# Performance work log

Measured on AMD Instinct MI355X. Metric: run time of the kernel, lower is better.

Reference implementation:

```python
import jax, jax.numpy as jnp
import numpy as np

H_SIZE = 768
N_HEADS = 12
HEAD = H_SIZE // N_HEADS
INTER = 3072
N_LAYERS = 6
VOCAB = 65536
WIDTH = 512  # attention_width
EPS = 1e-6


def rmsnorm(x, w):
    return x * jax.lax.rsqrt(jnp.mean(x * x, axis=-1, keepdims=True) + EPS) * w


def rotate_every_two(x):
    # interleaved rotation: (x0,x1,x2,x3,...) -> (-x1,x0,-x3,x2,...)
    x1 = x[..., ::2]
    x2 = x[..., 1::2]
    return jnp.stack((-x2, x1), axis=-1).reshape(x.shape)


def fixed_pos_embedding(ages, dim):
    # ages: [B,S] float32 -> sin,cos: [B,S,1,dim]
    inv_freq = 1.0 / 10000 ** jnp.linspace(0.0, 2.0, dim // 2)
    t = ages[..., None] * inv_freq  # [B,S,dim//2]
    sin, cos = jnp.sin(t), jnp.cos(t)
    shp = ages.shape + (1, dim)
    sin = jnp.stack((sin, sin), axis=-1).reshape(shp)
    cos = jnp.stack((cos, cos), axis=-1).reshape(shp)
    return sin, cos


def local_attention(q, k, v, width):
    # causal local attention: query i attends to keys j with i-width < j <= i
    B, S, H, D = q.shape
    nb = S // width
    qb = q.reshape(B, nb, width, H, D)
    pad = ((0, 0), (width, 0), (0, 0), (0, 0))
    kp = jnp.pad(k, pad).reshape(B, nb + 1, width, H, D)
    vp = jnp.pad(v, pad).reshape(B, nb + 1, width, H, D)
    k2 = jnp.concatenate((kp[:, :-1], kp[:, 1:]), axis=2)  # [B,nb,2W,H,D]
    v2 = jnp.concatenate((vp[:, :-1], vp[:, 1:]), axis=2)
    scale = 1.0 / jnp.sqrt(jnp.asarray(D, q.dtype))
    scores = jnp.einsum('bnqhd,bnkhd->bnhqk', qb, k2) * scale
    qi = jnp.arange(width)[:, None]
    kj = jnp.arange(2 * width)[None, :]
    blk = jnp.arange(nb)[:, None, None]
    # global: i = b*W+qi, j = b*W - W + kj ; valid: j<=i, i-j<W, j>=0
    valid = (kj > qi) & (kj <= qi + width) & ((blk * width - width + kj) >= 0)
    scores = jnp.where(valid[None, :, None, :, :], scores, -jnp.inf)
    attn = jax.nn.softmax(scores, axis=-1)
    out = jnp.einsum('bnhqk,bnkhd->bnqhd', attn, v2)
    return out.reshape(B, S, H, D)


def encoder_layer(x, sin, cos, p):
    B, S, _ = x.shape
    xn = rmsnorm(x, p['norm_w'])
    qkv = (xn @ p['attn_W'] + p['attn_b']).reshape(B, S, 3, N_HEADS, HEAD)
    q = qkv[:, :, 0] * cos + rotate_every_two(qkv[:, :, 0]) * sin
    k = qkv[:, :, 1] * cos + rotate_every_two(qkv[:, :, 1]) * sin
    v = qkv[:, :, 2]
    attn = local_attention(q, k, v, WIDTH).reshape(B, S, H_SIZE)
    ff = jax.nn.gelu(xn @ p['in_W'] + p['in_b'], approximate=False)
    combined = jnp.concatenate((attn, ff), axis=-1)
    return combined @ p['out_W'] + p['out_b']


def setup_inputs() -> dict:
    key = jax.random.key(0)
    ks = jax.random.split(key, 10)
    B, S = 4, 2048
    std = 0.02
    tokens = jax.random.randint(ks[0], (B, S), 0, VOCAB, dtype=jnp.int64 if jax.config.jax_enable_x64 else jnp.int32)
    ages = jax.random.uniform(ks[1], (B, S), dtype=jnp.float32) * 1000.0
    embed = jax.random.normal(ks[2], (VOCAB, H_SIZE), jnp.float32) * std
    in_norm_w = jnp.ones((H_SIZE,), jnp.float32)
    out_norm_w = jnp.ones((H_SIZE,), jnp.float32)
    norm_w = jnp.ones((N_LAYERS, H_SIZE), jnp.float32)
    attn_W = jax.random.normal(ks[3], (N_LAYERS, H_SIZE, 3 * H_SIZE), jnp.float32) * std
    attn_b = jnp.zeros((N_LAYERS, 3 * H_SIZE), jnp.float32)
    in_W = jax.random.normal(ks[4], (N_LAYERS, H_SIZE, INTER), jnp.float32) * std
    in_b = jnp.zeros((N_LAYERS, INTER), jnp.float32)
    out_W = jax.random.normal(ks[5], (N_LAYERS, H_SIZE + INTER, H_SIZE), jnp.float32) * std
    out_b = jnp.zeros((N_LAYERS, H_SIZE), jnp.float32)
    return {'tokens': tokens, 'ages': ages, 'embed': embed,
            'in_norm_w': in_norm_w, 'out_norm_w': out_norm_w, 'norm_w': norm_w,
            'attn_W': attn_W, 'attn_b': attn_b, 'in_W': in_W, 'in_b': in_b,
            'out_W': out_W, 'out_b': out_b}


def reference(tokens, ages, embed, in_norm_w, out_norm_w, norm_w, attn_W, attn_b, in_W, in_b, out_W, out_b):
    x = embed[tokens]
    x = rmsnorm(x, in_norm_w)
    sin, cos = fixed_pos_embedding(ages, HEAD)
    params = {'norm_w': norm_w, 'attn_W': attn_W, 'attn_b': attn_b,
              'in_W': in_W, 'in_b': in_b, 'out_W': out_W, 'out_b': out_b}

    def step(h, p):
        return h + encoder_layer(h, sin, cos, p), None

    x, _ = jax.lax.scan(step, x, params)
    return rmsnorm(x, out_norm_w)
```

## Files before the change

### kernel.cpp

```cpp
#include <hip/hip_runtime.h>
#include <hip/hip_bf16.h>
#include <math.h>

#define H_SIZE 768
#define N_HEADS 12
#define HEAD 64
#define INTER 3072
#define N_LAYERS 6
#define BATCH 4
#define SEQ 2048
#define BS (BATCH*SEQ)
#define EPSV 1e-6f

typedef __attribute__((ext_vector_type(8))) short bf16x8;
typedef __attribute__((ext_vector_type(4))) float f32x4;
typedef unsigned short u16;

__device__ inline float bf2f(u16 v) {
    union { float f; unsigned u; } x; x.u = ((unsigned)v) << 16; return x.f;
}
__device__ inline u16 f2bf(float f) {
    union { float f; unsigned u; } x; x.f = f;
    unsigned u = x.u;
    return (u16)((u + 0x7FFFu + ((u >> 16) & 1u)) >> 16);
}

__device__ __forceinline__ void stage16(const u16* g, u16* ldsbase) {
    __builtin_amdgcn_global_load_lds((const __attribute__((address_space(1))) void*)g,
                                     (__attribute__((address_space(3))) void*)ldsbase,
                                     16, 0, 0);
}

__global__ void probe_kernel(const u16* __restrict__ embed, const int* __restrict__ tokens,
                             int* __restrict__ flags) {
    if (threadIdx.x == 0 && blockIdx.x == 0) {
        int good = 0, evenzero = 0;
        for (int i = 0; i < 128; i++) {
            u16 h = embed[i];
            int e = (h >> 7) & 0xFF;
            if (h == 0 || (e >= 87 && e <= 133)) good++;
            if ((i & 1) == 0 && h == 0) evenzero++;
        }
        flags[0] = (evenzero >= 48) ? 1 : ((good >= 110) ? 0 : 1);
        int z = 0;
        for (int i = 0; i < 64; i++) if (tokens[2 * i + 1] == 0) z++;
        flags[1] = (z >= 60) ? 1 : 0;
    }
}

__global__ __launch_bounds__(256) void sincos_kernel(const void* __restrict__ ages,
                                                     float* __restrict__ SIN,
                                                     float* __restrict__ COS,
                                                     const int* __restrict__ flags) {
    int idx = blockIdx.x * 256 + threadIdx.x;
    if (idx >= BS * 32) return;
    bool f32in = flags[0] != 0;
    int row = idx >> 5, f = idx & 31;
    float age = f32in ? ((const float*)ages)[row] : bf2f(((const u16*)ages)[row]);
    float inv = expf(-(2.0f * (float)f / 31.0f) * 9.210340371976184f);
    float t = age * inv;
    SIN[idx] = sinf(t);
    COS[idx] = cosf(t);
}

__global__ __launch_bounds__(256) void wtrans_kernel(const void* __restrict__ Wsrc,
                                                     u16* __restrict__ Wt,
                                                     int K, int N, size_t ltstride,
                                                     const int* __restrict__ flags) {
    __shared__ u16 tile[64][72];
    bool f32in = flags[0] != 0;
    int l = blockIdx.z;
    const float* W32 = (const float*)Wsrc + (size_t)l * K * N;
    const u16*   W16 = (const u16*)Wsrc + (size_t)l * K * N;
    u16* out = Wt + (size_t)l * ltstride;
    int k0 = blockIdx.y * 64, n0 = blockIdx.x * 64;
    int t = threadIdx.x;
    int kk = t >> 3, nn = (t & 7) * 8;
#pragma unroll
    for (int it = 0; it < 2; it++) {
        int kr = kk + it * 32;
        u16 tmp[8];
        if (f32in) {
            const float* src = W32 + (size_t)(k0 + kr) * N + n0 + nn;
            float4 f0 = *(const float4*)src, f1 = *(const float4*)(src + 4);
            tmp[0] = f2bf(f0.x); tmp[1] = f2bf(f0.y); tmp[2] = f2bf(f0.z); tmp[3] = f2bf(f0.w);
            tmp[4] = f2bf(f1.x); tmp[5] = f2bf(f1.y); tmp[6] = f2bf(f1.z); tmp[7] = f2bf(f1.w);
        } else {
            uint4 v = *(const uint4*)(W16 + (size_t)(k0 + kr) * N + n0 + nn);
            const u16* pv = (const u16*)&v;
#pragma unroll
            for (int i = 0; i < 8; i++) tmp[i] = pv[i];
        }
        *(uint4*)(&tile[kr][nn]) = *(const uint4*)tmp;
    }
    __syncthreads();
    int n = t >> 3, kq = (t & 7) * 8;
#pragma unroll
    for (int it = 0; it < 2; it++) {
        int nr = n + it * 32;
        u16 tmp[8];
#pragma unroll
        for (int i = 0; i < 8; i++) tmp[i] = tile[kq + i][nr];
        *(uint4*)(out + (size_t)(n0 + nr) * K + k0 + kq) = *(const uint4*)tmp;
    }
}

__global__ __launch_bounds__(256) void bias_conv_kernel(const void* __restrict__ ab,
                                                        const void* __restrict__ ib,
                                                        const void* __restrict__ ob,
                                                        u16* __restrict__ dst,
                                                        const int* __restrict__ flags) {
    int i = blockIdx.x * 256 + threadIdx.x;
    bool f32in = flags[0] != 0;
    const int A = 6 * 2304, B = 6 * 3072, C = 6 * 768;
    if (i < A) dst[i] = f32in ? f2bf(((const float*)ab)[i]) : ((const u16*)ab)[i];
    else if (i < A + B) { int j = i - A; dst[i] = f32in ? f2bf(((const float*)ib)[j]) : ((const u16*)ib)[j]; }
    else if (i < A + B + C) { int j = i - A - B; dst[i] = f32in ? f2bf(((const float*)ob)[j]) : ((const u16*)ob)[j]; }
}

__global__ __launch_bounds__(256) void embed_norm_kernel(const int* __restrict__ tokens,
                                                         const void* __restrict__ embed,
                                                         const void* __restrict__ wbase,
                                                         float* __restrict__ X,
                                                         const int* __restrict__ flags) {
    int row = blockIdx.x * 4 + (threadIdx.x >> 6);
    int lane = threadIdx.x & 63;
    bool f32in = flags[0] != 0;
    bool i64 = flags[1] != 0;
    int tok = i64 ? tokens[2 * row] : tokens[row];
    tok &= 65535;
    const u16* er16 = (const u16*)embed + (size_t)tok * H_SIZE;
    const float* er32 = (const float*)embed + (size_t)tok * H_SIZE;
    const u16* w16 = (const u16*)wbase;
    const float* w32 = (const float*)wbase;
    float v[12]; float ss = 0.f;
#pragma unroll
    for (int k = 0; k < 12; k++) {
        int i = lane + k * 64;
        float t = f32in ? er32[i] : bf2f(er16[i]);
        v[k] = t; ss += t * t;
    }
#pragma unroll
    for (int off = 1; off < 64; off <<= 1) ss += __shfl_xor(ss, off, 64);
    float scale = rsqrtf(ss * (1.0f / 768.0f) + EPSV);
#pragma unroll
    for (int k = 0; k < 12; k++) {
        int i = lane + k * 64;
        float wv = f32in ? w32[i] : bf2f(w16[i]);
        X[(size_t)row * H_SIZE + i] = v[k] * scale * wv;
    }
}

__global__ __launch_bounds__(256) void rmsnorm_kernel(const float* __restrict__ X,
                                                      const void* __restrict__ wbase, size_t woff,
                                                      void* __restrict__ Y, int outMode,
                                                      const int* __restrict__ flags) {
    int row = blockIdx.x * 4 + (threadIdx.x >> 6);
    int lane = threadIdx.x & 63;
    bool f32in = flags[0] != 0;
    const u16* w16 = (const u16*)wbase + woff;
    const float* w32 = (const float*)wbase + woff;
    const float* xr = X + (size_t)row * H_SIZE;
    float v[12]; float ss = 0.f;
#pragma unroll
    for (int k = 0; k < 12; k++) { v[k] = xr[lane + k * 64]; ss += v[k] * v[k]; }
#pragma unroll
    for (int off = 1; off < 64; off <<= 1) ss += __shfl_xor(ss, off, 64);
    float scale = rsqrtf(ss * (1.0f / 768.0f) + EPSV);
    bool of32 = outMode && f32in;
#pragma unroll
    for (int k = 0; k < 12; k++) {
        int i = lane + k * 64;
        float wv = f32in ? w32[i] : bf2f(w16[i]);
        float val = v[k] * scale * wv;
        if (of32) ((float*)Y)[(size_t)row * H_SIZE + i] = val;
        else      ((u16*)Y)[(size_t)row * H_SIZE + i] = f2bf(val);
    }
}

template <int EPI, int BN, int MGRP>
__global__ __launch_bounds__(256) void gemm_kernel(const u16* __restrict__ A,
                                                   const u16* __restrict__ Wt,
                                                   const u16* __restrict__ abias,
                                                   const u16* __restrict__ bbias,
                                                   float* __restrict__ Cf,
                                                   u16* __restrict__ qkvb,
                                                   u16* __restrict__ combb,
                                                   int K,
                                                   const float* __restrict__ SIN,
                                                   const float* __restrict__ COS) {
    constexpr int NF = BN / 32;
    constexpr int LPS = (BN == 128) ? 4 : 3;
    __shared__ u16 Al[3][128][32];
    __shared__ u16 Bl[3][BN][32];
    const int tid = threadIdx.x;
    const int lane = tid & 63, wave = tid >> 6;
    const int wm = wave >> 1, wn = wave & 1;
    const int lm = lane & 15, g = lane >> 4;

    const int nx = gridDim.x;
    const int mpx = gridDim.y >> 3;
    int linear = blockIdx.y * nx + blockIdx.x;
    const int xcd = linear & 7;
    int wch = linear >> 3;
    const int grpsz = MGRP * nx;
    int grp = wch / grpsz;
    int rem = wch - grp * grpsz;
    int n_idx = rem / MGRP;
    int m_loc = grp * MGRP + (rem - n_idx * MGRP);
    const int m0 = (xcd * mpx + m_loc) * 128;
    const int n0 = n_idx * BN;

    f32x4 acc[4][NF];
#pragma unroll
    for (int i = 0; i < 4; i++)
#pragma unroll
        for (int j = 0; j < NF; j++) acc[i][j] = (f32x4)0.0f;

    const int swcol = ((lane & 3) ^ ((lane >> 3) & 3)) * 8;
    const u16* ga = A  + (size_t)(m0 + wave * 16 + (lane >> 2)) * K + swcol;
    const u16* gb = Wt + (size_t)(n0 + wave * 16 + (lane >> 2)) * K + swcol;
    const size_t row64 = (size_t)64 * K;

    auto STAGE = [&](int bi, int kk) {
        stage16(ga + kk, &Al[bi][wave * 16][0]);
        stage16(ga + row64 + kk, &Al[bi][64 + wave * 16][0]);
        stage16(gb + kk, &Bl[bi][wave * 16][0]);
        if constexpr (BN == 128) stage16(gb + row64 + kk, &Bl[bi][64 + wave * 16][0]);
    };

    const int cc = (g ^ ((lm >> 1) & 3)) * 8;

    auto BODY = [&](int BUF, int NXT, int T) {
        if (T + 32 < K) asm volatile("s_waitcnt vmcnt(%0)" :: "i"(LPS) : "memory");
        else            asm volatile("s_waitcnt vmcnt(0)" ::: "memory");
        __builtin_amdgcn_s_barrier();
        if (T + 64 < K) STAGE(NXT, T + 64);
        bf16x8 a[4], b[NF];
#pragma unroll
        for (int i = 0; i < 4; i++) a[i] = *(const bf16x8*)(&Al[BUF][wm * 64 + i * 16 + lm][cc]);
#pragma unroll
        for (int j = 0; j < NF; j++) b[j] = *(const bf16x8*)(&Bl[BUF][wn * (BN / 2) + j * 16 + lm][cc]);
        __builtin_amdgcn_s_setprio(1);
#pragma unroll
        for (int i = 0; i < 4; i++)
#pragma unroll
            for (int j = 0; j < NF; j++)
                acc[i][j] = __builtin_amdgcn_mfma_f32_16x16x32_bf16(a[i], b[j], acc[i][j], 0, 0, 0);
        __builtin_amdgcn_s_setprio(0);
    };

    STAGE(0, 0);
    STAGE(1, 32);
    for (int k0 = 0; k0 < K; k0 += 96) {
        BODY(0, 2, k0);
        BODY(1, 0, k0 + 32);
        BODY(2, 1, k0 + 64);
    }

#pragma unroll
    for (int i = 0; i < 4; i++) {
        int mbase = m0 + wm * 64 + i * 16 + g * 4;
#pragma unroll
        for (int j = 0; j < NF; j++) {
            int n = n0 + wn * (BN / 2) + j * 16 + lm;
            float bv;
            if (EPI == 0) bv = (n < 2304) ? bf2f(abias[n]) : bf2f(bbias[n - 2304]);
            else          bv = bf2f(abias[n]);
#pragma unroll
            for (int r = 0; r < 4; r++) {
                float v = acc[i][j][r] + bv;
                int mm = mbase + r;
                if (EPI == 0) {
                    float p = __shfl_xor(v, 1);
                    if (n < 2304) {
                        float outv = v;
                        if (n < 1536) {
                            int f = (n >> 1) & 31;
                            float c = COS[mm * 32 + f], s = SIN[mm * 32 + f];
                            outv = (n & 1) ? (v * c + p * s) : (v * c - p * s);
                        }
                        qkvb[(size_t)mm * 2304 + n] = f2bf(outv);
                    } else {
                        float u = 0.7978845608f * (v + 0.044715f * v * v * v);
                        float e = __expf(2.0f * u);
                        float th = 1.0f - 2.0f / (e + 1.0f);
                        combb[(size_t)mm * 3840 + (n - 1536)] = f2bf(0.5f * v * (1.0f + th));
                    }
                } else {
                    Cf[(size_t)mm * 768 + n] += v;
                }
            }
        }
    }
}

__global__ __launch_bounds__(512) void attn_kernel(const u16* __restrict__ qkv,
                                                   u16* __restrict__ Out) {
    __shared__ u16 Qs[128][72];
    __shared__ u16 Ks[64][72];
    __shared__ u16 Vt[64][72];
    __shared__ u16 Ps[8][16][72];

    const int tid = threadIdx.x;
    const int lane = tid & 63, wave = tid >> 6;
    const int lm = lane & 15, g = lane >> 4;
    const int q0 = blockIdx.x * 128;
    const int h = blockIdx.y;
    const int b = blockIdx.z;
    const size_t rowbase = (size_t)b * SEQ;

#pragma unroll
    for (int it = 0; it < 2; ++it) {
        int idx = tid + it * 512;
        int r = idx >> 3, u = (idx & 7) * 8;
        uint4 v = *(const uint4*)(qkv + (rowbase + q0 + r) * 2304 + h * HEAD + u);
        *(uint4*)(&Qs[r][u]) = v;
    }

    float m_r[4], l_r[4];
    f32x4 o[4];
#pragma unroll
    for (int r = 0; r < 4; r++) { m_r[r] = -INFINITY; l_r[r] = 0.f; }
#pragma unroll
    for (int d = 0; d < 4; d++) o[d] = (f32x4)0.0f;

    const int c_start = (q0 < 512) ? ((512 - q0) >> 6) : 0;
    for (int c = c_start; c < 10; ++c) {
        int kc = q0 - 512 + c * 64;
        __syncthreads();
        {
            int r = tid >> 3, u = (tid & 7) * 8;
            int j = kc + r;
            uint4 kv = make_uint4(0, 0, 0, 0), vv = make_uint4(0, 0, 0, 0);
            if (j >= 0) {
                kv = *(const uint4*)(qkv + (rowbase + j) * 2304 + 768 + h * HEAD + u);
                vv = *(const uint4*)(qkv + (rowbase + j) * 2304 + 1536 + h * HEAD + u);
            }
            *(uint4*)(&Ks[r][u]) = kv;
            const u16* pv = (const u16*)&vv;
#pragma unroll
            for (int i = 0; i < 8; i++) Vt[u + i][r] = pv[i];
        }
        __syncthreads();

        bf16x8 aq0 = *(const bf16x8*)(&Qs[wave * 16 + lm][g * 8]);
        bf16x8 aq1 = *(const bf16x8*)(&Qs[wave * 16 + lm][32 + g * 8]);
        f32x4 s[4];
#pragma unroll
        for (int kf = 0; kf < 4; kf++) {
            bf16x8 b0 = *(const bf16x8*)(&Ks[kf * 16 + lm][g * 8]);
            bf16x8 b1 = *(const bf16x8*)(&Ks[kf * 16 + lm][32 + g * 8]);
            f32x4 z = (f32x4)0.0f;
            z = __builtin_amdgcn_mfma_f32_16x16x32_bf16(aq0, b0, z, 0, 0, 0);
            z = __builtin_amdgcn_mfma_f32_16x16x32_bf16(aq1, b1, z, 0, 0, 0);
            s[kf] = z;
        }

        float sv[4][4], mc[4];
#pragma unroll
        for (int r = 0; r < 4; r++) mc[r] = -INFINITY;
#pragma unroll
        for (int kf = 0; kf < 4; kf++) {
            int j = kc + kf * 16 + lm;
#pragma unroll
            for (int r = 0; r < 4; r++) {
                int i = q0 + wave * 16 + g * 4 + r;
                bool valid = (j >= 0) && (j <= i) && (j >= i - 511);
                float v = valid ? s[kf][r] * 0.125f : -INFINITY;
                sv[kf][r] = v;
                mc[r] = fmaxf(mc[r], v);
            }
        }
#pragma unroll
        for (int off = 1; off < 16; off <<= 1)
#pragma unroll
            for (int r = 0; r < 4; r++) mc[r] = fmaxf(mc[r], __shfl_xor(mc[r], off, 64));

        float alpha[4], mn[4];
#pragma unroll
        for (int r = 0; r < 4; r++) {
            mn[r] = fmaxf(m_r[r], mc[r]);
            alpha[r] = (mn[r] > -1e37f) ? __expf(m_r[r] - mn[r]) : 1.0f;
            m_r[r] = mn[r];
        }
        float ps[4][4], rs[4] = {0.f, 0.f, 0.f, 0.f};
#pragma unroll
        for (int kf = 0; kf < 4; kf++)
#pragma unroll
            for (int r = 0; r < 4; r++) {
                float p = (sv[kf][r] > -1e37f) ? __expf(sv[kf][r] - mn[r]) : 0.0f;
                ps[kf][r] = p;
                rs[r] += p;
            }
#pragma unroll
        for (int off = 1; off < 16; off <<= 1)
#pragma unroll
            for (int r = 0; r < 4; r++) rs[r] += __shfl_xor(rs[r], off, 64);
#pragma unroll
        for (int r = 0; r < 4; r++) l_r[r] = l_r[r] * alpha[r] + rs[r];

#pragma unroll
        for (int kf = 0; kf < 4; kf++)
#pragma unroll
            for (int r = 0; r < 4; r++) Ps[wave][g * 4 + r][kf * 16 + lm] = f2bf(ps[kf][r]);

#pragma unroll
        for (int d = 0; d < 4; d++)
#pragma unroll
            for (int r = 0; r < 4; r++) o[d][r] *= alpha[r];

        bf16x8 pa0 = *(const bf16x8*)(&Ps[wave][lm][g * 8]);
        bf16x8 pa1 = *(const bf16x8*)(&Ps[wave][lm][32 + g * 8]);
#pragma unroll
        for (int d = 0; d < 4; d++) {
            bf16x8 b0 = *(const bf16x8*)(&Vt[d * 16 + lm][g * 8]);
            bf16x8 b1 = *(const bf16x8*)(&Vt[d * 16 + lm][32 + g * 8]);
            o[d] = __builtin_amdgcn_mfma_f32_16x16x32_bf16(pa0, b0, o[d], 0, 0, 0);
            o[d] = __builtin_amdgcn_mfma_f32_16x16x32_bf16(pa1, b1, o[d], 0, 0, 0);
        }
    }

#pragma unroll
    for (int d = 0; d < 4; d++) {
        int dd = d * 16 + lm;
#pragma unroll
        for (int r = 0; r < 4; r++) {
            int i = q0 + wave * 16 + g * 4 + r;
            float v = o[d][r] / l_r[r];
            Out[(rowbase + i) * 3840 + h * HEAD + dd] = f2bf(v);
        }
    }
}

extern "C" void kernel_launch(void* const* d_in, const int* in_sizes, int n_in,
                              void* d_out, int out_size, void* d_ws, size_t ws_size,
                              hipStream_t stream) {
    const int* tokens   = (const int*)d_in[0];
    const void* ages    = d_in[1];
    const void* embed   = d_in[2];
    const void* in_norm_w  = d_in[3];
    const void* out_norm_w = d_in[4];
    const void* norm_w     = d_in[5];
    const void* attn_W     = d_in[6];
    const void* attn_b     = d_in[7];
    const void* in_W       = d_in[8];
    const void* in_b       = d_in[9];
    const void* out_W      = d_in[10];
    const void* out_b      = d_in[11];

    char* w = (char*)d_ws;
    int* flags  = (int*)w;   w += 256;
    float* x    = (float*)w; w += (size_t)BS * H_SIZE * 4;
    u16* xn     = (u16*)w;   w += (size_t)BS * H_SIZE * 2;
    u16* qkv    = (u16*)w;   w += (size_t)BS * 2304 * 2;
    u16* comb   = (u16*)w;   w += (size_t)BS * 3840 * 2;
    float* sinb = (float*)w; w += (size_t)BS * 32 * 4;
    float* cosb = (float*)w; w += (size_t)BS * 32 * 4;
    u16* wtf    = (u16*)w;   w += (size_t)N_LAYERS * 5376 * 768 * 2;
    u16* wto    = (u16*)w;   w += (size_t)N_LAYERS * 768 * 3840 * 2;
    u16* biasb  = (u16*)w;   w += (size_t)(6*2304 + 6*3072 + 6*768) * 2;

    u16* ab_b = biasb;
    u16* ib_b = biasb + 6 * 2304;
    u16* ob_b = ib_b + 6 * 3072;

    const size_t LFS = (size_t)5376 * 768;

    probe_kernel<<<1, 64, 0, stream>>>((const u16*)embed, tokens, flags);
    sincos_kernel<<<(BS * 32 + 255) / 256, 256, 0, stream>>>(ages, sinb, cosb, flags);
    embed_norm_kernel<<<BS / 4, 256, 0, stream>>>(tokens, embed, in_norm_w, x, flags);
    bias_conv_kernel<<<(6 * (2304 + 3072 + 768) + 255) / 256, 256, 0, stream>>>(
        attn_b, in_b, out_b, biasb, flags);

    wtrans_kernel<<<dim3(2304 / 64, 768 / 64, N_LAYERS), 256, 0, stream>>>(
        attn_W, wtf, 768, 2304, LFS, flags);
    wtrans_kernel<<<dim3(3072 / 64, 768 / 64, N_LAYERS), 256, 0, stream>>>(
        in_W, wtf + (size_t)2304 * 768, 768, 3072, LFS, flags);
    wtrans_kernel<<<dim3(768 / 64, 3840 / 64, N_LAYERS), 256, 0, stream>>>(
        out_W, wto, 3840, 768, (size_t)768 * 3840, flags);

    for (int l = 0; l < N_LAYERS; ++l) {
        rmsnorm_kernel<<<BS / 4, 256, 0, stream>>>(x, norm_w, (size_t)l * H_SIZE, xn, 0, flags);
        gemm_kernel<0, 128, 8><<<dim3(5376 / 128, BS / 128), 256, 0, stream>>>(
            xn, wtf + (size_t)l * LFS, ab_b + l * 2304, ib_b + l * 3072,
            nullptr, qkv, comb, H_SIZE, sinb, cosb);
        attn_kernel<<<dim3(SEQ / 128, N_HEADS, BATCH), 512, 0, stream>>>(qkv, comb);
        gemm_kernel<2, 64, 2><<<dim3(768 / 64, BS / 128), 256, 0, stream>>>(
            comb, wto + (size_t)l * 768 * 3840, ob_b + l * 768, nullptr,
            x, nullptr, nullptr, H_SIZE + INTER, nullptr, nullptr);
    }
    rmsnorm_kernel<<<BS / 4, 256, 0, stream>>>(x, out_norm_w, 0, d_out, 1, flags);
}
```

Baseline: 1.772 ms.

## Add 256x256-tile 8-wave GEMM for fused QKV/FFN-in projection

Replaces the 128x128-tile, 4-wave GEMM used for the fused QKV plus FFN-input projection with a dedicated 256x256-tile, 512-thread kernel. It uses BK=64, double-buffered XOR-swizzled LDS and a four-quarter compute schedule that interleaves next-tile staging with MFMA sub-blocks, separated by barriers. The larger tile raises arithmetic intensity and cuts global reloads of A and B. The cost is about 128 KB of LDS per block and heavy register pressure from 32 accumulators per lane. The grid shrinks to 21x32 blocks, which gives fewer blocks for occupancy and load balance. The output-projection GEMM is split out unchanged apart from a simplified epilogue.

```diff
diff --git a/kernel.cpp b/kernel.cpp
--- a/kernel.cpp
+++ b/kernel.cpp
@@ -178,17 +178,154 @@
     }
 }
 
-template <int EPI, int BN, int MGRP>
-__global__ __launch_bounds__(256) void gemm_kernel(const u16* __restrict__ A,
-                                                   const u16* __restrict__ Wt,
-                                                   const u16* __restrict__ abias,
-                                                   const u16* __restrict__ bbias,
-                                                   float* __restrict__ Cf,
-                                                   u16* __restrict__ qkvb,
-                                                   u16* __restrict__ combb,
-                                                   int K,
-                                                   const float* __restrict__ SIN,
-                                                   const float* __restrict__ COS) {
+__global__ __launch_bounds__(512, 2)
+void gemm_fused_kernel(const u16* __restrict__ A,
+                       const u16* __restrict__ Wt,
+                       const u16* __restrict__ abias,
+                       const u16* __restrict__ bbias,
+                       u16* __restrict__ qkvb,
+                       u16* __restrict__ combb,
+                       const float* __restrict__ SIN,
+                       const float* __restrict__ COS) {
+    const int K = H_SIZE;
+    const int NT = K / 64;
+    __shared__ u16 Al[2][256][64];
+    __shared__ u16 Bl[2][256][64];
+    const int tid = threadIdx.x;
+    const int lane = tid & 63, wave = tid >> 6;
+    const int wm = wave >> 2, wn = wave & 3;
+    const int lm = lane & 15, g = lane >> 4;
+    const int l8 = lane >> 3, l7 = lane & 7;
+
+    const int nx = gridDim.x;
+    const int mpx = gridDim.y >> 3;
+    int linear = blockIdx.y * nx + blockIdx.x;
+    const int xcd = linear & 7;
+    int wch = linear >> 3;
+    int n_idx = wch / mpx;
+    int m_loc = wch - n_idx * mpx;
+    const int m0 = (xcd * mpx + m_loc) * 256;
+    const int n0 = n_idx * 256;
+
+    f32x4 acc[8][4];
+#pragma unroll
+    for (int i = 0; i < 8; i++)
+#pragma unroll
+        for (int j = 0; j < 4; j++) acc[i][j] = (f32x4)0.0f;
+
+    const int swc = (l7 ^ l8) * 8;
+    const u16* gA = A  + (size_t)(m0 + wave * 8 + l8) * K + swc;
+    const u16* gB = Wt + (size_t)(n0 + wave * 8 + l8) * K + swc;
+
+    auto STAGE_HALF = [&](int bi, int t, int which) {
+        int h = (which & 1) * 128;
+        if (which < 2) {
+            stage16(gA + (size_t)h * K + t * 64,        &Al[bi][h + wave * 8][0]);
+            stage16(gA + (size_t)(h + 64) * K + t * 64, &Al[bi][h + wave * 8 + 64][0]);
+        } else {
+            stage16(gB + (size_t)h * K + t * 64,        &Bl[bi][h + wave * 8][0]);
+            stage16(gB + (size_t)(h + 64) * K + t * 64, &Bl[bi][h + wave * 8 + 64][0]);
+        }
+    };
+
+    bf16x8 af[4][2], bf[4][2];
+    const int rowsw = (lm & 7);
+
+    auto RD_A = [&](int bi, int mh) {
+#pragma unroll
+        for (int i = 0; i < 4; i++)
+#pragma unroll
+            for (int ks = 0; ks < 2; ks++)
+                af[i][ks] = *(const bf16x8*)(&Al[bi][wm * 128 + mh * 64 + i * 16 + lm]
+                                               [((ks * 4 + g) ^ rowsw) * 8]);
+    };
+    auto RD_B = [&](int bi, int nh) {
+#pragma unroll
+        for (int j = 0; j < 2; j++)
+#pragma unroll
+            for (int ks = 0; ks < 2; ks++)
+                bf[nh * 2 + j][ks] = *(const bf16x8*)(&Bl[bi][wn * 64 + nh * 32 + j * 16 + lm]
+                                                        [((ks * 4 + g) ^ rowsw) * 8]);
+    };
+    auto MM = [&](int mh, int nh) {
+        __builtin_amdgcn_s_setprio(1);
+#pragma unroll
+        for (int i = 0; i < 4; i++)
+#pragma unroll
+            for (int j = 0; j < 2; j++)
+#pragma unroll
+                for (int ks = 0; ks < 2; ks++)
+                    acc[mh * 4 + i][nh * 2 + j] = __builtin_amdgcn_mfma_f32_16x16x32_bf16(
+                        af[i][ks], bf[nh * 2 + j][ks], acc[mh * 4 + i][nh * 2 + j], 0, 0, 0);
+        __builtin_amdgcn_s_setprio(0);
+    };
+
+    STAGE_HALF(0, 0, 0); STAGE_HALF(0, 0, 1); STAGE_HALF(0, 0, 2); STAGE_HALF(0, 0, 3);
+
+    auto ITER = [&](int t, int ct) {
+        const int nb = ct ^ 1;
+        const bool pf = (t + 1 < NT);
+        asm volatile("s_waitcnt vmcnt(0)" ::: "memory");
+        __builtin_amdgcn_s_barrier();
+        if (pf) STAGE_HALF(nb, t + 1, 0);
+        RD_A(ct, 0); RD_B(ct, 0);
+        MM(0, 0);
+        __builtin_amdgcn_s_barrier();
+        if (pf) STAGE_HALF(nb, t + 1, 1);
+        RD_B(ct, 1);
+        MM(0, 1);
+        __builtin_amdgcn_s_barrier();
+        if (pf) STAGE_HALF(nb, t + 1, 2);
+        RD_A(ct, 1);
+        MM(1, 0);
+        __builtin_amdgcn_s_barrier();
+        if (pf) STAGE_HALF(nb, t + 1, 3);
+        MM(1, 1);
+        __builtin_amdgcn_s_barrier();
+    };
+
+    for (int tt = 0; tt < NT; tt += 2) {
+        ITER(tt, 0);
+        ITER(tt + 1, 1);
+    }
+
+#pragma unroll
+    for (int i = 0; i < 8; i++) {
+        int mbase = m0 + wm * 128 + i * 16 + g * 4;
+#pragma unroll
+        for (int j = 0; j < 4; j++) {
+            int n = n0 + wn * 64 + j * 16 + lm;
+            float bv = (n < 2304) ? bf2f(abias[n]) : bf2f(bbias[n - 2304]);
+#pragma unroll
+            for (int r = 0; r < 4; r++) {
+                float v = acc[i][j][r] + bv;
+                int mm = mbase + r;
+                float p = __shfl_xor(v, 1);
+                if (n < 2304) {
+                    float outv = v;
+                    if (n < 1536) {
+                        int f = (n >> 1) & 31;
+                        float c = COS[mm * 32 + f], s = SIN[mm * 32 + f];
+                        outv = (n & 1) ? (v * c + p * s) : (v * c - p * s);
+                    }
+                    qkvb[(size_t)mm * 2304 + n] = f2bf(outv);
+                } else {
+                    float u = 0.7978845608f * (v + 0.044715f * v * v * v);
+                    float e = __expf(2.0f * u);
+                    float th = 1.0f - 2.0f / (e + 1.0f);
+                    combb[(size_t)mm * 3840 + (n - 1536)] = f2bf(0.5f * v * (1.0f + th));
+                }
+            }
+        }
+    }
+}
+
+template <int BN, int MGRP>
+__global__ __launch_bounds__(256) void gemm_out_kernel(const u16* __restrict__ A,
+                                                       const u16* __restrict__ Wt,
+                                                       const u16* __restrict__ bias,
+                                                       float* __restrict__ Cf,
+                                                       int K) {
     constexpr int NF = BN / 32;
     constexpr int LPS = (BN == 128) ? 4 : 3;
     __shared__ u16 Al[3][128][32];
@@ -264,32 +401,12 @@
 #pragma unroll
         for (int j = 0; j < NF; j++) {
             int n = n0 + wn * (BN / 2) + j * 16 + lm;
-            float bv;
-            if (EPI == 0) bv = (n < 2304) ? bf2f(abias[n]) : bf2f(bbias[n - 2304]);
-            else          bv = bf2f(abias[n]);
+            float bv = bf2f(bias[n]);
 #pragma unroll
             for (int r = 0; r < 4; r++) {
                 float v = acc[i][j][r] + bv;
                 int mm = mbase + r;
-                if (EPI == 0) {
-                    float p = __shfl_xor(v, 1);
-                    if (n < 2304) {
-                        float outv = v;
-                        if (n < 1536) {
-                            int f = (n >> 1) & 31;
-                            float c = COS[mm * 32 + f], s = SIN[mm * 32 + f];
-                            outv = (n & 1) ? (v * c + p * s) : (v * c - p * s);
-                        }
-                        qkvb[(size_t)mm * 2304 + n] = f2bf(outv);
-                    } else {
-                        float u = 0.7978845608f * (v + 0.044715f * v * v * v);
-                        float e = __expf(2.0f * u);
-                        float th = 1.0f - 2.0f / (e + 1.0f);
-                        combb[(size_t)mm * 3840 + (n - 1536)] = f2bf(0.5f * v * (1.0f + th));
-                    }
-                } else {
-                    Cf[(size_t)mm * 768 + n] += v;
-                }
+                Cf[(size_t)mm * 768 + n] += v;
             }
         }
     }
@@ -482,13 +599,12 @@
 
     for (int l = 0; l < N_LAYERS; ++l) {
         rmsnorm_kernel<<<BS / 4, 256, 0, stream>>>(x, norm_w, (size_t)l * H_SIZE, xn, 0, flags);
-        gemm_kernel<0, 128, 8><<<dim3(5376 / 128, BS / 128), 256, 0, stream>>>(
+        gemm_fused_kernel<<<dim3(5376 / 256, BS / 256), 512, 0, stream>>>(
             xn, wtf + (size_t)l * LFS, ab_b + l * 2304, ib_b + l * 3072,
-            nullptr, qkv, comb, H_SIZE, sinb, cosb);
+            qkv, comb, sinb, cosb);
         attn_kernel<<<dim3(SEQ / 128, N_HEADS, BATCH), 512, 0, stream>>>(qkv, comb);
-        gemm_kernel<2, 64, 2><<<dim3(768 / 64, BS / 128), 256, 0, stream>>>(
-            comb, wto + (size_t)l * 768 * 3840, ob_b + l * 768, nullptr,
-            x, nullptr, nullptr, H_SIZE + INTER, nullptr, nullptr);
+        gemm_out_kernel<64, 2><<<dim3(768 / 64, BS / 128), 256, 0, stream>>>(
+            comb, wto + (size_t)l * 768 * 3840, ob_b + l * 768, x, H_SIZE + INTER);
     }
     rmsnorm_kernel<<<BS / 4, 256, 0, stream>>>(x, out_norm_w, 0, d_out, 1, flags);
 }
```

Result: slower. 1.905 ms (+7.5%).

## Load GEMM A operand directly from global into registers, bypassing LDS

Applied to the files above, without the earlier changes.

The A tile is no longer staged through shared memory. Each wave loads its MFMA A fragments straight from global memory into double-buffered registers, one k-step ahead, while B keeps the triple-buffered LDS pipeline. The loop is unrolled to six steps so the register buffers alternate, and the vmcnt waits are adjusted to match. This removes LDS traffic and capacity for A, but the global loads are less coalesced, A reuse across the two N-waves is lost, and register pressure rises.

```diff
diff --git a/kernel.cpp b/kernel.cpp
--- a/kernel.cpp
+++ b/kernel.cpp
@@ -190,8 +190,7 @@
                                                    const float* __restrict__ SIN,
                                                    const float* __restrict__ COS) {
     constexpr int NF = BN / 32;
-    constexpr int LPS = (BN == 128) ? 4 : 3;
-    __shared__ u16 Al[3][128][32];
+    constexpr int VC = (BN == 128) ? 6 : 5;
     __shared__ u16 Bl[3][BN][32];
     const int tid = threadIdx.x;
     const int lane = tid & 63, wave = tid >> 6;
@@ -218,45 +217,65 @@
         for (int j = 0; j < NF; j++) acc[i][j] = (f32x4)0.0f;
 
     const int swcol = ((lane & 3) ^ ((lane >> 3) & 3)) * 8;
-    const u16* ga = A  + (size_t)(m0 + wave * 16 + (lane >> 2)) * K + swcol;
     const u16* gb = Wt + (size_t)(n0 + wave * 16 + (lane >> 2)) * K + swcol;
     const size_t row64 = (size_t)64 * K;
 
-    auto STAGE = [&](int bi, int kk) {
-        stage16(ga + kk, &Al[bi][wave * 16][0]);
-        stage16(ga + row64 + kk, &Al[bi][64 + wave * 16][0]);
-        stage16(gb + kk, &Bl[bi][wave * 16][0]);
-        if constexpr (BN == 128) stage16(gb + row64 + kk, &Bl[bi][64 + wave * 16][0]);
-    };
+    const u16* aP0 = A + (size_t)(m0 + wm * 64 + lm) * K + g * 8;
+    const u16* aP1 = aP0 + (size_t)16 * K;
+    const u16* aP2 = aP1 + (size_t)16 * K;
+    const u16* aP3 = aP2 + (size_t)16 * K;
+
+    bf16x8 afA[4], afB[4];
+
+#define LOAD_A(AF, T) do {                         \
+        AF[0] = *(const bf16x8*)(aP0 + (T));       \
+        AF[1] = *(const bf16x8*)(aP1 + (T));       \
+        AF[2] = *(const bf16x8*)(aP2 + (T));       \
+        AF[3] = *(const bf16x8*)(aP3 + (T));       \
+    } while (0)
+
+#define STAGE_B(BI, KK) do {                                          \
+        stage16(gb + (KK), &Bl[BI][wave * 16][0]);                    \
+        if (BN == 128) stage16(gb + row64 + (KK), &Bl[BI][64 + wave * 16][0]); \
+    } while (0)
 
     const int cc = (g ^ ((lm >> 1) & 3)) * 8;
 
-    auto BODY = [&](int BUF, int NXT, int T) {
-        if (T + 32 < K) asm volatile("s_waitcnt vmcnt(%0)" :: "i"(LPS) : "memory");
-        else            asm volatile("s_waitcnt vmcnt(0)" ::: "memory");
-        __builtin_amdgcn_s_barrier();
-        if (T + 64 < K) STAGE(NXT, T + 64);
-        bf16x8 a[4], b[NF];
-#pragma unroll
-        for (int i = 0; i < 4; i++) a[i] = *(const bf16x8*)(&Al[BUF][wm * 64 + i * 16 + lm][cc]);
-#pragma unroll
-        for (int j = 0; j < NF; j++) b[j] = *(const bf16x8*)(&Bl[BUF][wn * (BN / 2) + j * 16 + lm][cc]);
-        __builtin_amdgcn_s_setprio(1);
-#pragma unroll
-        for (int i = 0; i < 4; i++)
-#pragma unroll
-            for (int j = 0; j < NF; j++)
-                acc[i][j] = __builtin_amdgcn_mfma_f32_16x16x32_bf16(a[i], b[j], acc[i][j], 0, 0, 0);
-        __builtin_amdgcn_s_setprio(0);
-    };
-
-    STAGE(0, 0);
-    STAGE(1, 32);
-    for (int k0 = 0; k0 < K; k0 += 96) {
-        BODY(0, 2, k0);
-        BODY(1, 0, k0 + 32);
-        BODY(2, 1, k0 + 64);
-    }
+#define GBODY(BUF, NXT, AFC, AFN, T) do {                                         \
+        if ((T) + 32 < K) { asm volatile("s_waitcnt vmcnt(%0)" :: "i"(VC) : "memory"); } \
+        else              { asm volatile("s_waitcnt vmcnt(4)" ::: "memory"); }    \
+        __builtin_amdgcn_s_barrier();                                             \
+        if ((T) + 32 < K) LOAD_A(AFN, (T) + 32);                                  \
+        if ((T) + 64 < K) STAGE_B(NXT, (T) + 64);                                 \
+        bf16x8 b[NF];                                                             \
+        _Pragma("unroll")                                                         \
+        for (int j = 0; j < NF; j++)                                              \
+            b[j] = *(const bf16x8*)(&Bl[BUF][wn * (BN / 2) + j * 16 + lm][cc]);   \
+        __builtin_amdgcn_s_setprio(1);                                            \
+        _Pragma("unroll")                                                         \
+        for (int i = 0; i < 4; i++)                                               \
+            _Pragma("unroll")                                                     \
+            for (int j = 0; j < NF; j++)                                          \
+                acc[i][j] = __builtin_amdgcn_mfma_f32_16x16x32_bf16(AFC[i], b[j], acc[i][j], 0, 0, 0); \
+        __builtin_amdgcn_s_setprio(0);                                            \
+    } while (0)
+
+    STAGE_B(0, 0);
+    LOAD_A(afA, 0);
+    STAGE_B(1, 32);
+
+    for (int k0 = 0; k0 < K; k0 += 192) {
+        GBODY(0, 2, afA, afB, k0);
+        GBODY(1, 0, afB, afA, k0 + 32);
+        GBODY(2, 1, afA, afB, k0 + 64);
+        GBODY(0, 2, afB, afA, k0 + 96);
+        GBODY(1, 0, afA, afB, k0 + 128);
+        GBODY(2, 1, afB, afA, k0 + 160);
+    }
+
+#undef GBODY
+#undef STAGE_B
+#undef LOAD_A
 
 #pragma unroll
     for (int i = 0; i < 4; i++) {
```

Measured after the change: 2.724 ms. +53.7%, slower.
